# Performance work log

Measured on AMD Instinct MI355X. Metric: run time of the kernel, lower is better.

Reference implementation:

```python
import jax, jax.numpy as jnp
import numpy as np

B, L = 16, 256
H, NH, NL = 512, 8, 6
NTOK = 10000
P, K = 4, 9          # parser layers, conv kernel size
DFF = 4 * H


def layernorm(x, s=None, b=None, eps=1e-5):
    m = x.mean(-1, keepdims=True)
    v = ((x - m) ** 2).mean(-1, keepdims=True)
    y = (x - m) * jax.lax.rsqrt(v + eps)
    if s is not None:
        y = y * s + b
    return y


def conv1d(h, w, b):
    # h: (B,L,C); w: (K,Cin,Cout); 'same' padding (K odd)
    pad = (K - 1) // 2
    return jax.lax.conv_general_dilated(
        h, w, (1,), [(pad, pad)], dimension_numbers=('NWC', 'WIO', 'NWC')) + b


def setup_inputs():
    key = jax.random.key(0)
    ks = iter(jax.random.split(key, 40))
    r = lambda shape, s=0.02: jax.random.normal(next(ks), shape, jnp.float32) * s
    return dict(
        x=jax.random.randint(next(ks), (B, L), 0, NTOK, jnp.int32),
        pos=jnp.tile(jnp.arange(L, dtype=jnp.int32), (B, 1)),
        emb=r((NTOK, H), 0.1),
        conv_w=r((P, K, H, H)), conv_b=jnp.zeros((P, H)),
        parent_w=r((H, H)), parent_b=jnp.zeros((H,)),
        child_w=r((H, H)), child_b=jnp.zeros((H,)),
        rel_w_param=r((NL, NH, 2), 0.1),
        qkv_w=r((NL, 3 * H, H)), qkv_b=jnp.zeros((NL, 3 * H)),
        out_w=r((NL, H, H)), out_b=jnp.zeros((NL, H)),
        ln1_s=jnp.ones((NL, H)), ln1_b=jnp.zeros((NL, H)),
        ln2_s=jnp.ones((NL, H)), ln2_b=jnp.zeros((NL, H)),
        ff1_w=r((NL, DFF, H)), ff1_b=jnp.zeros((NL, DFF)),
        ff2_w=r((NL, H, DFF)), ff2_b=jnp.zeros((NL, H)),
        norm_s=jnp.ones((H,)), norm_b=jnp.zeros((H,)),
        out_bias=jnp.zeros((NTOK,)),
    )


def _forward(x, floats):
    (emb, conv_w, conv_b, parent_w, parent_b, child_w, child_b, rel_w_param,
     qkv_w, qkv_b, out_w, out_b, ln1_s, ln1_b, ln2_s, ln2_b,
     ff1_w, ff1_b, ff2_w, ff2_b, norm_s, norm_b, out_bias) = floats
    mask = x != 0  # pad token index = 0
    DH = H // NH
    scale = H ** -0.5
    # ---- differentiable parser: Conv1d + LN(no affine) + Tanh stack ----
    h = emb[x]
    for i in range(P):
        h = jnp.where(mask[..., None], h, 0.0)
        h = jnp.tanh(layernorm(conv1d(h, conv_w[i], conv_b[i])))
    parent = h @ parent_w.T + parent_b
    child = h @ child_w.T + child_b
    logits = jnp.einsum('bid,bjd->bij', child, parent) * scale
    logits = jnp.where(mask[:, None, :], logits, -jnp.inf)
    # NB: source applies scaling twice (masked_fill then softmax(logits*scaling))
    p = jax.nn.softmax(logits * scale, axis=-1)  # (B,L,L) head distribution
    # ---- structural relations -> per-layer/per-head attention bias ----
    eye = jnp.eye(L, dtype=bool)
    head = jnp.where(eye, 0.0, p)
    child_rel = jnp.swapaxes(head, 1, 2)
    rel = jnp.stack([head, child_rel], axis=1)            # (B,2,L,L)
    rel_weight = jax.nn.softmax(rel_w_param, axis=-1)     # (NL,NH,2)
    dep = jnp.einsum('lhr,brij->lbhij', rel_weight, rel)  # (NL,B,NH,L,L)
    # ---- pre-LN transformer encoder with structural bias injection ----
    logvis = jnp.where(mask, 0.0, -jnp.inf)[:, None, None, :]  # key padding mask (log)
    h = emb[x]
    for i in range(NL):
        hn = layernorm(h, ln1_s[i], ln1_b[i])
        qkv = hn @ qkv_w[i].T + qkv_b[i]
        q, k, v = jnp.split(qkv, 3, axis=-1)
        split = lambda t: t.reshape(B, L, NH, DH).transpose(0, 2, 1, 3)
        q, k, v = split(q), split(k), split(v)
        att = jnp.einsum('bhid,bhjd->bhij', q, k) * (DH ** -0.5) + dep[i] + logvis
        att = jax.nn.softmax(att, axis=-1)
        ctx = jnp.einsum('bhij,bhjd->bhid', att, v).transpose(0, 2, 1, 3).reshape(B, L, H)
        h = h + ctx @ out_w[i].T + out_b[i]
        hn = layernorm(h, ln2_s[i], ln2_b[i])
        h = h + jax.nn.leaky_relu(hn @ ff1_w[i].T + ff1_b[i], 0.01) @ ff2_w[i].T + ff2_b[i]
    raw = layernorm(h, norm_s, norm_b)
    out = (raw @ emb.T + out_bias).reshape(B * L, NTOK)  # tied output embedding
    return out


def reference(x, pos, emb, conv_w, conv_b, parent_w, parent_b, child_w, child_b,
              rel_w_param, qkv_w, qkv_b, out_w, out_b, ln1_s, ln1_b, ln2_s, ln2_b,
              ff1_w, ff1_b, ff2_w, ff2_b, norm_s, norm_b, out_bias):
    floats = (emb, conv_w, conv_b, parent_w, parent_b, child_w, child_b, rel_w_param,
              qkv_w, qkv_b, out_w, out_b, ln1_s, ln1_b, ln2_s, ln2_b,
              ff1_w, ff1_b, ff2_w, ff2_b, norm_s, norm_b, out_bias)
    return _forward(x, floats)
```

## Files before the change

kernel.cpp:

```cpp
#include <hip/hip_runtime.h>
#include <hip/hip_bf16.h>


typedef unsigned short u16;
typedef unsigned char  u8;
typedef short short8 __attribute__((ext_vector_type(8)));
typedef float f32x4  __attribute__((ext_vector_type(4)));

static constexpr int CB=16, CL=256, CH=512, CNH=8, CDH=64, CNL=6;
static constexpr int CNTOK=10000, CP=4, CKS=9, CDFF=2048, CT=CB*CL;

__device__ __forceinline__ u16 f2b(float x){
    union { float f; unsigned u; } v; v.f = x;
    unsigned r = v.u + 0x7fffu + ((v.u >> 16) & 1u);
    return (u16)(r >> 16);
}
__device__ __forceinline__ float b2f(u16 u){
    union { unsigned u; float f; } v; v.u = ((unsigned)u) << 16; return v.f;
}
__device__ __forceinline__ unsigned pack2(float a, float b){
    return (unsigned)f2b(a) | ((unsigned)f2b(b) << 16);
}

template<bool OBF>
__global__ __launch_bounds__(256) void embed_k(const int* __restrict__ x,
    const float* __restrict__ emb, void* __restrict__ out, u8* __restrict__ mask)
{
    int t = blockIdx.x, tid = threadIdx.x;
    int tok = x[t];
    if (tid == 0) mask[t] = (tok != 0) ? 1 : 0;
    const float* e = emb + (size_t)tok * CH;
    if (OBF) {
        u16* o = (u16*)out + (size_t)t * CH;
        o[tid] = f2b(e[tid]); o[tid + 256] = f2b(e[tid + 256]);
    } else {
        float* o = (float*)out + (size_t)t * CH;
        o[tid] = e[tid]; o[tid + 256] = e[tid + 256];
    }
}

template<bool INBF, bool AFFINE, bool DOTANH>
__global__ __launch_bounds__(256) void ln_k(const void* __restrict__ in,
    const float* __restrict__ s, const float* __restrict__ b, u16* __restrict__ out)
{
    int t = blockIdx.x, tid = threadIdx.x;
    float x0, x1;
    if (INBF) {
        const u16* row = (const u16*)in + (size_t)t * CH;
        x0 = b2f(row[tid]); x1 = b2f(row[tid + 256]);
    } else {
        const float* row = (const float*)in + (size_t)t * CH;
        x0 = row[tid]; x1 = row[tid + 256];
    }
    float sum = x0 + x1, sq = x0*x0 + x1*x1;
    #pragma unroll
    for (int o = 32; o; o >>= 1) { sum += __shfl_down(sum, o); sq += __shfl_down(sq, o); }
    __shared__ float rs[4], rq[4];
    int w = tid >> 6, lane = tid & 63;
    if (lane == 0) { rs[w] = sum; rq[w] = sq; }
    __syncthreads();
    sum = rs[0] + rs[1] + rs[2] + rs[3];
    sq  = rq[0] + rq[1] + rq[2] + rq[3];
    float mean = sum * (1.f/512.f);
    float var  = fmaxf(sq * (1.f/512.f) - mean*mean, 0.f);
    float rstd = rsqrtf(var + 1e-5f);
    float y0 = (x0 - mean) * rstd, y1 = (x1 - mean) * rstd;
    if (AFFINE) {
        y0 = y0 * s[tid]       + b[tid];
        y1 = y1 * s[tid + 256] + b[tid + 256];
    }
    if (DOTANH) { y0 = tanhf(y0); y1 = tanhf(y1); }
    u16* o = out + (size_t)t * CH;
    o[tid] = f2b(y0); o[tid + 256] = f2b(y1);
}

__global__ __launch_bounds__(256) void tp_conv(const float* __restrict__ src,
    u16* __restrict__ dst)
{
    __shared__ float tile[32][33];
    int z = blockIdx.z, p = z / 9, t = z % 9;
    int ci0 = blockIdx.y * 32, co0 = blockIdx.x * 32;
    int tx = threadIdx.x, ty = threadIdx.y;
    #pragma unroll
    for (int yy = 0; yy < 4; yy++) {
        int i = ty + yy*8;
        tile[i][tx] = src[((size_t)z*512 + ci0 + i)*512 + co0 + tx];
    }
    __syncthreads();
    #pragma unroll
    for (int yy = 0; yy < 4; yy++) {
        int i = ty + yy*8;
        dst[((size_t)p*512 + co0 + i)*4608 + (size_t)t*512 + ci0 + tx] = f2b(tile[tx][i]);
    }
}

template<bool CONV, int BSRC, int ACT, int OUT, int BMT>
__global__ __launch_bounds__(256) void gemm_mfma(
    const u16* __restrict__ A, const void* __restrict__ Bv,
    const float* __restrict__ bias, void* __restrict__ Cv,
    const u8* __restrict__ mask,
    int M, int N, int K, float alpha, long sA, long sB, long sC)
{
    constexpr int BM = BMT, MI = BMT/32;
    __shared__ __align__(16) u16 Al[4][BM][8];
    __shared__ __align__(16) u16 Bl[4][128][8];
    const int tid  = threadIdx.x;
    const int lane = tid & 63, wave = tid >> 6;
    const int q = lane >> 4, ln = lane & 15;
    const int wm = wave >> 1, wn = wave & 1;
    const int m0 = blockIdx.y * BM, n0 = blockIdx.x * 128;
    const int z  = blockIdx.z;
    A += (size_t)z * sA;

    f32x4 acc[MI][4];
    #pragma unroll
    for (int i = 0; i < MI; i++)
        #pragma unroll
        for (int j = 0; j < 4; j++)
            #pragma unroll
            for (int r = 0; r < 4; r++) acc[i][j][r] = 0.f;

    int ar, ak;
    if (BMT == 128) { ar = tid >> 1; ak = (tid & 1) * 16; }
    else            { ar = tid >> 2; ak = (tid & 3) * 8;  }
    const int br = tid >> 1, bk = (tid & 1) * 16;
    const int bn = n0 + br;

    const float* Bf = (const float*)Bv;
    const u16*   Bb = (const u16*)Bv;
    if (BSRC == 0) Bf += (size_t)z * sB; else Bb += (size_t)z * sB;

    for (int k0 = 0; k0 < K; k0 += 32) {
        {
            int row = m0 + ar;
            const u16* src;
            bool ok = true;
            if (CONV) {
                int koff = k0 >> 9;
                int ci   = (k0 & 511) + ak;
                int bb   = row >> 8;
                int l2   = (row & 255) + koff - 4;
                ok = ((unsigned)l2 < 256u) && mask[(bb << 8) | l2];
                src = A + ((size_t)((bb << 8) | l2)) * CH + ci;
            } else {
                src = A + (size_t)row * K + k0 + ak;
            }
            uint4 zv; zv.x = zv.y = zv.z = zv.w = 0u;
            if (BMT == 128) {
                uint4 v0 = ok ? *(const uint4*)src       : zv;
                uint4 v1 = ok ? *(const uint4*)(src + 8) : zv;
                int kq = (tid & 1) * 2;
                *(uint4*)&Al[kq][ar][0]     = v0;
                *(uint4*)&Al[kq + 1][ar][0] = v1;
            } else {
                uint4 v0 = ok ? *(const uint4*)src : zv;
                *(uint4*)&Al[tid & 3][ar][0] = v0;
            }
        }
        {
            uint4 w0, w1;
            w0.x = w0.y = w0.z = w0.w = 0u;
            w1 = w0;
            if (bn < N) {
                if (BSRC == 0) {
                    const float* s = Bf + (size_t)bn * K + k0 + bk;
                    float4 f0 = *(const float4*)s;
                    float4 f1 = *(const float4*)(s + 4);
                    float4 f2 = *(const float4*)(s + 8);
                    float4 f3 = *(const float4*)(s + 12);
                    w0.x = pack2(f0.x, f0.y); w0.y = pack2(f0.z, f0.w);
                    w0.z = pack2(f1.x, f1.y); w0.w = pack2(f1.z, f1.w);
                    w1.x = pack2(f2.x, f2.y); w1.y = pack2(f2.z, f2.w);
                    w1.z = pack2(f3.x, f3.y); w1.w = pack2(f3.z, f3.w);
                } else {
                    const u16* s = Bb + (size_t)bn * K + k0 + bk;
                    w0 = *(const uint4*)s;
                    w1 = *(const uint4*)(s + 8);
                }
            }
            int kq = (tid & 1) * 2;
            *(uint4*)&Bl[kq][br][0]     = w0;
            *(uint4*)&Bl[kq + 1][br][0] = w1;
        }
        __syncthreads();
        short8 af[MI], bf[4];
        #pragma unroll
        for (int i = 0; i < MI; i++)
            af[i] = *(const short8*)&Al[q][wm*(BM/2) + i*16 + ln][0];
        #pragma unroll
        for (int j = 0; j < 4; j++)
            bf[j] = *(const short8*)&Bl[q][wn*64 + j*16 + ln][0];
        #pragma unroll
        for (int i = 0; i < MI; i++)
            #pragma unroll
            for (int j = 0; j < 4; j++)
                acc[i][j] = __builtin_amdgcn_mfma_f32_16x16x32_bf16(af[i], bf[j], acc[i][j], 0, 0, 0);
        __syncthreads();
    }
    float* Cf = (float*)Cv; u16* Cb = (u16*)Cv;
    #pragma unroll
    for (int i = 0; i < MI; i++) {
        int row0 = m0 + wm*(BM/2) + i*16 + q*4;
        #pragma unroll
        for (int j = 0; j < 4; j++) {
            int col = n0 + wn*64 + j*16 + ln;
            if (col < N) {
                #pragma unroll
                for (int r = 0; r < 4; r++) {
                    float v = acc[i][j][r] * alpha;
                    if (bias) v += bias[col];
                    if (ACT == 1) v = v > 0.f ? v : 0.01f * v;
                    size_t idx = (size_t)z * sC + (size_t)(row0 + r) * N + col;
                    if (OUT == 0)      Cf[idx] = v;
                    else if (OUT == 1) Cb[idx] = f2b(v);
                    else               Cf[idx] += v;
                }
            }
        }
    }
}

__global__ __launch_bounds__(256) void softmax_head(float* __restrict__ sc,
    const u8* __restrict__ mask)
{
    int bi = blockIdx.x;
    int b = bi >> 8, i = bi & 255;
    int j = threadIdx.x;
    float* rowp = sc + (size_t)bi * CL;
    bool valid = mask[(b << 8) | j] != 0;
    float v = valid ? rowp[j] : -1e30f;
    float mx = v;
    #pragma unroll
    for (int o = 32; o; o >>= 1) mx = fmaxf(mx, __shfl_down(mx, o));
    __shared__ float rm[4], rsum[4];
    int w = j >> 6, lane = j & 63;
    if (lane == 0) rm[w] = mx;
    __syncthreads();
    mx = fmaxf(fmaxf(rm[0], rm[1]), fmaxf(rm[2], rm[3]));
    float e = valid ? __expf(v - mx) : 0.f;
    float ssum = e;
    #pragma unroll
    for (int o = 32; o; o >>= 1) ssum += __shfl_down(ssum, o);
    if (lane == 0) rsum[w] = ssum;
    __syncthreads();
    ssum = rsum[0] + rsum[1] + rsum[2] + rsum[3];
    float r = e / fmaxf(ssum, 1e-30f);
    if (j == i) r = 0.f;
    rowp[j] = r;
}

__global__ __launch_bounds__(256) void attn_k(const u16* __restrict__ qkv,
    const float* __restrict__ head, const float* __restrict__ relw,
    const u8* __restrict__ mask, u16* __restrict__ ctx, int layer)
{
    __shared__ __align__(16) u16 Ks[CL * CDH];
    __shared__ __align__(16) u16 Vs[CL * CDH];
    int bx = blockIdx.x;
    int b = bx >> 4, hd = (bx >> 1) & 7, qh = bx & 1;
    int tid = threadIdx.x;

    #pragma unroll
    for (int r = 0; r < 8; r++) {
        int ef = tid + 256 * r;
        int j = ef >> 3, d8 = (ef & 7) * 8;
        const u16* ps = qkv + (size_t)(b*256 + j) * 1536 + 512 + hd*64 + d8;
        *(uint4*)&Ks[j*64 + d8] = *(const uint4*)ps;
        *(uint4*)&Vs[j*64 + d8] = *(const uint4*)(ps + 512);
    }

    int qi = qh * 128 + (tid >> 1);
    int half = tid & 1;
    float qv[CDH];
    {
        const u16* qp = qkv + (size_t)(b*256 + qi) * 1536 + hd*64;
        #pragma unroll
        for (int c = 0; c < 8; c++) {
            uint4 u = *(const uint4*)(qp + c*8);
            unsigned uu[4] = {u.x, u.y, u.z, u.w};
            #pragma unroll
            for (int p2 = 0; p2 < 4; p2++) {
                qv[c*8 + p2*2]     = b2f((u16)(uu[p2] & 0xffffu));
                qv[c*8 + p2*2 + 1] = b2f((u16)(uu[p2] >> 16));
            }
        }
    }
    float r0 = relw[((layer << 3) + hd) * 2 + 0];
    float r1 = relw[((layer << 3) + hd) * 2 + 1];
    float e0 = __expf(r0), e1 = __expf(r1);
    float w0 = e0 / (e0 + e1), w1 = 1.f - w0;

    __syncthreads();

    const float* h1 = head + ((size_t)b << 16) + ((size_t)qi << 8);
    const float* h2 = head + ((size_t)b << 16) + qi;
    const u8* mb = mask + (b << 8);

    float m = -1e30f, lsum = 0.f;
    float acc[CDH];
    #pragma unroll
    for (int d = 0; d < CDH; d++) acc[d] = 0.f;

    for (int jj = 0; jj < 128; jj++) {
        int j = half * 128 + jj;
        if (!mb[j]) continue;
        float dot = 0.f;
        #pragma unroll
        for (int d = 0; d < CDH; d++) dot += qv[d] * b2f(Ks[(j << 6) + d]);
        float s = dot * 0.125f + w0 * h1[j] + w1 * h2[(size_t)j << 8];
        float mn = fmaxf(m, s);
        float c = __expf(m - mn);
        float p = __expf(s - mn);
        lsum = lsum * c + p;
        #pragma unroll
        for (int d = 0; d < CDH; d++) acc[d] = acc[d] * c + p * b2f(Vs[(j << 6) + d]);
        m = mn;
    }
    {
        float mo = __shfl_xor(m, 1);
        float lo = __shfl_xor(lsum, 1);
        float M  = fmaxf(m, mo);
        float cs = __expf(m - M);
        float co = __expf(mo - M);
        lsum = lsum * cs + lo * co;
        #pragma unroll
        for (int d = 0; d < CDH; d++) {
            float ao = __shfl_xor(acc[d], 1);
            acc[d] = acc[d] * cs + ao * co;
        }
    }
    if (half == 0) {
        float inv = 1.f / fmaxf(lsum, 1e-30f);
        u16* cp = ctx + (size_t)(b*256 + qi) * CH + (hd << 6);
        #pragma unroll
        for (int d = 0; d < CDH; d++) cp[d] = f2b(acc[d] * inv);
    }
}

extern "C" void kernel_launch(void* const* d_in, const int* in_sizes, int n_in,
                              void* d_out, int out_size, void* d_ws, size_t ws_size,
                              hipStream_t stream)
{
    const int*   x        = (const int*)d_in[0];
    const float* emb      = (const float*)d_in[2];
    const float* conv_w   = (const float*)d_in[3];
    const float* conv_b   = (const float*)d_in[4];
    const float* parent_w = (const float*)d_in[5];
    const float* parent_b = (const float*)d_in[6];
    const float* child_w  = (const float*)d_in[7];
    const float* child_b  = (const float*)d_in[8];
    const float* rel_w    = (const float*)d_in[9];
    const float* qkv_w    = (const float*)d_in[10];
    const float* qkv_b    = (const float*)d_in[11];
    const float* out_w    = (const float*)d_in[12];
    const float* out_b    = (const float*)d_in[13];
    const float* ln1_s    = (const float*)d_in[14];
    const float* ln1_b    = (const float*)d_in[15];
    const float* ln2_s    = (const float*)d_in[16];
    const float* ln2_b    = (const float*)d_in[17];
    const float* ff1_w    = (const float*)d_in[18];
    const float* ff1_b    = (const float*)d_in[19];
    const float* ff2_w    = (const float*)d_in[20];
    const float* ff2_b    = (const float*)d_in[21];
    const float* norm_s   = (const float*)d_in[22];
    const float* norm_b   = (const float*)d_in[23];
    const float* out_bias = (const float*)d_in[24];

    float* ws = (float*)d_ws;
    float* h      = ws;
    float* headp  = ws + 2097152;
    u16*   abuf   = (u16*)(ws + 3145728);
    u16*   Rb     = (u16*)(ws + 4194304);
    u16*   qkvb   = Rb;
    u16*   parentb= Rb;
    u16*   childb = Rb + 2097152;
    u16*   convo  = Rb + 4194304;
    u16*   ctxb   = (u16*)(ws + 7340032);
    u16*   ff1b   = (u16*)(ws + 8388608);
    u16*   convwb = (u16*)(ws + 7340032);
    u8*    maskb  = (u8*)(ws + 12582912);

    tp_conv<<<dim3(16,16,36), dim3(32,8), 0, stream>>>(conv_w, convwb);

    embed_k<true><<<CT, 256, 0, stream>>>(x, emb, abuf, maskb);
    for (int p = 0; p < CP; p++) {
        gemm_mfma<true,1,0,1,64><<<dim3(4,64,1), 256, 0, stream>>>(
            abuf, convwb + (size_t)p*512*4608, conv_b + p*512, convo, maskb,
            CT, 512, 4608, 1.f, 0, 0, 0);
        ln_k<true,false,true><<<CT, 256, 0, stream>>>(convo, nullptr, nullptr, abuf);
    }
    gemm_mfma<false,0,0,1,64><<<dim3(4,64,1), 256, 0, stream>>>(
        abuf, parent_w, parent_b, parentb, nullptr, CT, 512, 512, 1.f, 0, 0, 0);
    gemm_mfma<false,0,0,1,64><<<dim3(4,64,1), 256, 0, stream>>>(
        abuf, child_w, child_b, childb, nullptr, CT, 512, 512, 1.f, 0, 0, 0);
    gemm_mfma<false,1,0,0,64><<<dim3(2,4,16), 256, 0, stream>>>(
        childb, parentb, nullptr, headp, nullptr, 256, 256, 512, 1.f/512.f,
        131072, 131072, 65536);
    softmax_head<<<CT, 256, 0, stream>>>(headp, maskb);

    embed_k<false><<<CT, 256, 0, stream>>>(x, emb, h, maskb);
    for (int l = 0; l < CNL; l++) {
        ln_k<false,true,false><<<CT, 256, 0, stream>>>(h, ln1_s + l*CH, ln1_b + l*CH, abuf);
        gemm_mfma<false,0,0,1,128><<<dim3(12,32,1), 256, 0, stream>>>(
            abuf, qkv_w + (size_t)l*1536*512, qkv_b + l*1536, qkvb, nullptr,
            CT, 1536, 512, 1.f, 0, 0, 0);
        attn_k<<<256, 256, 0, stream>>>(qkvb, headp, rel_w, maskb, ctxb, l);
        gemm_mfma<false,0,0,2,64><<<dim3(4,64,1), 256, 0, stream>>>(
            ctxb, out_w + (size_t)l*512*512, out_b + l*512, h, nullptr,
            CT, 512, 512, 1.f, 0, 0, 0);
        ln_k<false,true,false><<<CT, 256, 0, stream>>>(h, ln2_s + l*CH, ln2_b + l*CH, abuf);
        gemm_mfma<false,0,1,1,128><<<dim3(16,32,1), 256, 0, stream>>>(
            abuf, ff1_w + (size_t)l*2048*512, ff1_b + l*2048, ff1b, nullptr,
            CT, 2048, 512, 1.f, 0, 0, 0);
        gemm_mfma<false,0,0,2,64><<<dim3(4,64,1), 256, 0, stream>>>(
            ff1b, ff2_w + (size_t)l*512*2048, ff2_b + l*512, h, nullptr,
            CT, 512, 2048, 1.f, 0, 0, 0);
    }
    ln_k<false,true,false><<<CT, 256, 0, stream>>>(h, norm_s, norm_b, abuf);
    gemm_mfma<false,0,0,0,128><<<dim3(79,32,1), 256, 0, stream>>>(
        abuf, emb, out_bias, d_out, nullptr, CT, CNTOK, 512, 1.f, 0, 0, 0);
}
```

Before: 2.900 ms.

## Pre-convert weights to bf16 and load GEMM tiles via global_load_lds

Adds conversion kernels that turn all fp32 weight matrices and the tied embedding into bf16 copies once per call, padding the embedding to a multiple of 128 rows. The GEMM kernel is rewritten to stage A and B tiles straight into LDS with global_load_lds, replacing the register round trip and the per-tile fp32-to-bf16 packing. It also merges the two embedding gathers into one kernel and adds an optional workgroup swizzle, used for the output projection. The cost is extra conversion launches and extra memory traffic for the weight copies on every call.

```diff
diff --git a/kernel.cpp b/kernel.cpp
--- a/kernel.cpp
+++ b/kernel.cpp
@@ -9,6 +9,7 @@
 
 static constexpr int CB=16, CL=256, CH=512, CNH=8, CDH=64, CNL=6;
 static constexpr int CNTOK=10000, CP=4, CKS=9, CDFF=2048, CT=CB*CL;
+static constexpr int NTOKP=10112;
 
 __device__ __forceinline__ u16 f2b(float x){
     union { float f; unsigned u; } v; v.f = x;
@@ -21,22 +22,40 @@
 __device__ __forceinline__ unsigned pack2(float a, float b){
     return (unsigned)f2b(a) | ((unsigned)f2b(b) << 16);
 }
-
-template<bool OBF>
-__global__ __launch_bounds__(256) void embed_k(const int* __restrict__ x,
-    const float* __restrict__ emb, void* __restrict__ out, u8* __restrict__ mask)
+__device__ __forceinline__ void gll16(const void* g, void* l){
+    __builtin_amdgcn_global_load_lds(
+        (__attribute__((address_space(1))) void*)g,
+        (__attribute__((address_space(3))) void*)l, 16, 0, 0);
+}
+
+__global__ __launch_bounds__(256) void cvt_k(const float* __restrict__ in,
+    u16* __restrict__ out, long n, long total)
+{
+    long i = ((long)blockIdx.x * 256 + threadIdx.x) * 8;
+    if (i >= total) return;
+    uint4 o;
+    if (i < n) {
+        float4 a = *(const float4*)(in + i);
+        float4 b = *(const float4*)(in + i + 4);
+        o.x = pack2(a.x, a.y); o.y = pack2(a.z, a.w);
+        o.z = pack2(b.x, b.y); o.w = pack2(b.z, b.w);
+    } else { o.x = o.y = o.z = o.w = 0u; }
+    *(uint4*)(out + i) = o;
+}
+
+__global__ __launch_bounds__(256) void embed2_k(const int* __restrict__ x,
+    const float* __restrict__ emb, float* __restrict__ h,
+    u16* __restrict__ abuf, u8* __restrict__ maskb)
 {
     int t = blockIdx.x, tid = threadIdx.x;
     int tok = x[t];
-    if (tid == 0) mask[t] = (tok != 0) ? 1 : 0;
+    if (tid == 0) maskb[t] = (tok != 0) ? 1 : 0;
     const float* e = emb + (size_t)tok * CH;
-    if (OBF) {
-        u16* o = (u16*)out + (size_t)t * CH;
-        o[tid] = f2b(e[tid]); o[tid + 256] = f2b(e[tid + 256]);
-    } else {
-        float* o = (float*)out + (size_t)t * CH;
-        o[tid] = e[tid]; o[tid + 256] = e[tid + 256];
-    }
+    float v0 = e[tid], v1 = e[tid + 256];
+    float* hp = h + (size_t)t * CH;
+    hp[tid] = v0; hp[tid + 256] = v1;
+    u16* ap = abuf + (size_t)t * CH;
+    ap[tid] = f2b(v0); ap[tid + 256] = f2b(v1);
 }
 
 template<bool INBF, bool AFFINE, bool DOTANH>
@@ -94,23 +113,31 @@
     }
 }
 
-template<bool CONV, int BSRC, int ACT, int OUT, int BMT>
-__global__ __launch_bounds__(256) void gemm_mfma(
-    const u16* __restrict__ A, const void* __restrict__ Bv,
+template<int BM, bool CONV, int ACT, int OUT>
+__global__ __launch_bounds__(256) void gemm2(
+    const u16* __restrict__ A, const u16* __restrict__ B,
     const float* __restrict__ bias, void* __restrict__ Cv,
     const u8* __restrict__ mask,
-    int M, int N, int K, float alpha, long sA, long sB, long sC)
-{
-    constexpr int BM = BMT, MI = BMT/32;
-    __shared__ __align__(16) u16 Al[4][BM][8];
-    __shared__ __align__(16) u16 Bl[4][128][8];
+    int M, int N, int K, float alpha, long sA, long sB, long sC, int swz)
+{
+    constexpr int MI = BM / 32;
+    __shared__ __align__(16) u16 As[32 * BM];
+    __shared__ __align__(16) u16 Bs[4096];
+
+    int bx = blockIdx.x, by = blockIdx.y;
+    if (swz) {
+        int nwg = gridDim.x * gridDim.y;
+        int bid = by * gridDim.x + bx;
+        int s = (bid & 7) * (nwg >> 3) + (bid >> 3);
+        bx = s % gridDim.x; by = s / gridDim.x;
+    }
     const int tid  = threadIdx.x;
     const int lane = tid & 63, wave = tid >> 6;
     const int q = lane >> 4, ln = lane & 15;
     const int wm = wave >> 1, wn = wave & 1;
-    const int m0 = blockIdx.y * BM, n0 = blockIdx.x * 128;
+    const int m0 = by * BM, n0 = bx * 128;
     const int z  = blockIdx.z;
-    A += (size_t)z * sA;
+    A += (size_t)z * sA; B += (size_t)z * sB;
 
     f32x4 acc[MI][4];
     #pragma unroll
@@ -120,94 +147,61 @@
             #pragma unroll
             for (int r = 0; r < 4; r++) acc[i][j][r] = 0.f;
 
-    int ar, ak;
-    if (BMT == 128) { ar = tid >> 1; ak = (tid & 1) * 16; }
-    else            { ar = tid >> 2; ak = (tid & 3) * 8;  }
-    const int br = tid >> 1, bk = (tid & 1) * 16;
-    const int bn = n0 + br;
-
-    const float* Bf = (const float*)Bv;
-    const u16*   Bb = (const u16*)Bv;
-    if (BSRC == 0) Bf += (size_t)z * sB; else Bb += (size_t)z * sB;
-
     for (int k0 = 0; k0 < K; k0 += 32) {
-        {
-            int row = m0 + ar;
-            const u16* src;
-            bool ok = true;
-            if (CONV) {
-                int koff = k0 >> 9;
-                int ci   = (k0 & 511) + ak;
-                int bb   = row >> 8;
-                int l2   = (row & 255) + koff - 4;
-                ok = ((unsigned)l2 < 256u) && mask[(bb << 8) | l2];
-                src = A + ((size_t)((bb << 8) | l2)) * CH + ci;
+        if (!CONV) {
+            if (BM == 128) {
+                #pragma unroll
+                for (int t = 0; t < 2; t++) {
+                    int c = wave + t*4;
+                    int kq = c >> 1, rh = (c & 1) << 6;
+                    gll16(A + (size_t)(m0 + rh + lane) * K + k0 + kq*8, As + c*512);
+                }
             } else {
-                src = A + (size_t)row * K + k0 + ak;
+                gll16(A + (size_t)(m0 + lane) * K + k0 + wave*8, As + wave*512);
             }
-            uint4 zv; zv.x = zv.y = zv.z = zv.w = 0u;
-            if (BMT == 128) {
-                uint4 v0 = ok ? *(const uint4*)src       : zv;
-                uint4 v1 = ok ? *(const uint4*)(src + 8) : zv;
-                int kq = (tid & 1) * 2;
-                *(uint4*)&Al[kq][ar][0]     = v0;
-                *(uint4*)&Al[kq + 1][ar][0] = v1;
-            } else {
-                uint4 v0 = ok ? *(const uint4*)src : zv;
-                *(uint4*)&Al[tid & 3][ar][0] = v0;
-            }
+        } else {
+            int tap = k0 >> 9;
+            int ci  = (k0 & 511) + wave*8;
+            int gr  = m0 + lane;
+            int bb  = gr >> 8;
+            int l2  = (gr & 255) + tap - 4;
+            bool ok = ((unsigned)l2 < 256u) && mask[(bb << 8) | l2];
+            uint4 v; v.x = v.y = v.z = v.w = 0u;
+            if (ok) v = *(const uint4*)(A + ((size_t)((bb << 8) | l2)) * CH + ci);
+            *(uint4*)&As[wave*512 + lane*8] = v;
         }
-        {
-            uint4 w0, w1;
-            w0.x = w0.y = w0.z = w0.w = 0u;
-            w1 = w0;
-            if (bn < N) {
-                if (BSRC == 0) {
-                    const float* s = Bf + (size_t)bn * K + k0 + bk;
-                    float4 f0 = *(const float4*)s;
-                    float4 f1 = *(const float4*)(s + 4);
-                    float4 f2 = *(const float4*)(s + 8);
-                    float4 f3 = *(const float4*)(s + 12);
-                    w0.x = pack2(f0.x, f0.y); w0.y = pack2(f0.z, f0.w);
-                    w0.z = pack2(f1.x, f1.y); w0.w = pack2(f1.z, f1.w);
-                    w1.x = pack2(f2.x, f2.y); w1.y = pack2(f2.z, f2.w);
-                    w1.z = pack2(f3.x, f3.y); w1.w = pack2(f3.z, f3.w);
-                } else {
-                    const u16* s = Bb + (size_t)bn * K + k0 + bk;
-                    w0 = *(const uint4*)s;
-                    w1 = *(const uint4*)(s + 8);
-                }
-            }
-            int kq = (tid & 1) * 2;
-            *(uint4*)&Bl[kq][br][0]     = w0;
-            *(uint4*)&Bl[kq + 1][br][0] = w1;
+        #pragma unroll
+        for (int t = 0; t < 2; t++) {
+            int c = wave + t*4;
+            int kq = c >> 1, rh = (c & 1) << 6;
+            gll16(B + (size_t)(n0 + rh + lane) * K + k0 + kq*8, Bs + c*512);
         }
         __syncthreads();
         short8 af[MI], bf[4];
         #pragma unroll
-        for (int i = 0; i < MI; i++)
-            af[i] = *(const short8*)&Al[q][wm*(BM/2) + i*16 + ln][0];
-        #pragma unroll
-        for (int j = 0; j < 4; j++)
-            bf[j] = *(const short8*)&Bl[q][wn*64 + j*16 + ln][0];
-        #pragma unroll
-        for (int i = 0; i < MI; i++)
+        for (int f = 0; f < MI; f++)
+            af[f] = *(const short8*)&As[q*(BM*8) + (wm*(BM/2) + f*16 + ln)*8];
+        #pragma unroll
+        for (int g = 0; g < 4; g++)
+            bf[g] = *(const short8*)&Bs[q*1024 + (wn*64 + g*16 + ln)*8];
+        #pragma unroll
+        for (int f = 0; f < MI; f++)
             #pragma unroll
-            for (int j = 0; j < 4; j++)
-                acc[i][j] = __builtin_amdgcn_mfma_f32_16x16x32_bf16(af[i], bf[j], acc[i][j], 0, 0, 0);
+            for (int g = 0; g < 4; g++)
+                acc[f][g] = __builtin_amdgcn_mfma_f32_16x16x32_bf16(af[f], bf[g], acc[f][g], 0, 0, 0);
         __syncthreads();
     }
     float* Cf = (float*)Cv; u16* Cb = (u16*)Cv;
     #pragma unroll
-    for (int i = 0; i < MI; i++) {
-        int row0 = m0 + wm*(BM/2) + i*16 + q*4;
-        #pragma unroll
-        for (int j = 0; j < 4; j++) {
-            int col = n0 + wn*64 + j*16 + ln;
+    for (int f = 0; f < MI; f++) {
+        int row0 = m0 + wm*(BM/2) + f*16 + q*4;
+        #pragma unroll
+        for (int g = 0; g < 4; g++) {
+            int col = n0 + wn*64 + g*16 + ln;
             if (col < N) {
                 #pragma unroll
                 for (int r = 0; r < 4; r++) {
-                    float v = acc[i][j][r] * alpha;
+                    float v = acc[f][g][r] * alpha;
                     if (bias) v += bias[col];
                     if (ACT == 1) v = v > 0.f ? v : 0.01f * v;
                     size_t idx = (size_t)z * sC + (size_t)(row0 + r) * N + col;
@@ -378,44 +372,58 @@
     u16*   ff1b   = (u16*)(ws + 8388608);
     u16*   convwb = (u16*)(ws + 7340032);
     u8*    maskb  = (u8*)(ws + 12582912);
+    u16*   ebf16  = (u16*)(ws + 12583936);
+    u16*   qkvwb  = (u16*)(ws + 15172608);
+    u16*   outwb  = (u16*)(ws + 17531904);
+    u16*   ff1wb  = (u16*)(ws + 18318336);
+    u16*   ff2wb  = (u16*)(ws + 21464064);
+    u16*   parwb  = (u16*)(ws + 24609792);
+    u16*   chlwb  = (u16*)(ws + 24740864);
 
     tp_conv<<<dim3(16,16,36), dim3(32,8), 0, stream>>>(conv_w, convwb);
-
-    embed_k<true><<<CT, 256, 0, stream>>>(x, emb, abuf, maskb);
+    cvt_k<<<2528, 256, 0, stream>>>(emb,      ebf16, (long)CNTOK*CH, (long)NTOKP*CH);
+    cvt_k<<<2304, 256, 0, stream>>>(qkv_w,    qkvwb, 4718592L, 4718592L);
+    cvt_k<<< 768, 256, 0, stream>>>(out_w,    outwb, 1572864L, 1572864L);
+    cvt_k<<<3072, 256, 0, stream>>>(ff1_w,    ff1wb, 6291456L, 6291456L);
+    cvt_k<<<3072, 256, 0, stream>>>(ff2_w,    ff2wb, 6291456L, 6291456L);
+    cvt_k<<< 128, 256, 0, stream>>>(parent_w, parwb,  262144L,  262144L);
+    cvt_k<<< 128, 256, 0, stream>>>(child_w,  chlwb,  262144L,  262144L);
+
+    embed2_k<<<CT, 256, 0, stream>>>(x, emb, h, abuf, maskb);
+
     for (int p = 0; p < CP; p++) {
-        gemm_mfma<true,1,0,1,64><<<dim3(4,64,1), 256, 0, stream>>>(
+        gemm2<64,true,0,1><<<dim3(4,64,1), 256, 0, stream>>>(
             abuf, convwb + (size_t)p*512*4608, conv_b + p*512, convo, maskb,
-            CT, 512, 4608, 1.f, 0, 0, 0);
+            CT, 512, 4608, 1.f, 0, 0, 0, 0);
         ln_k<true,false,true><<<CT, 256, 0, stream>>>(convo, nullptr, nullptr, abuf);
     }
-    gemm_mfma<false,0,0,1,64><<<dim3(4,64,1), 256, 0, stream>>>(
-        abuf, parent_w, parent_b, parentb, nullptr, CT, 512, 512, 1.f, 0, 0, 0);
-    gemm_mfma<false,0,0,1,64><<<dim3(4,64,1), 256, 0, stream>>>(
-        abuf, child_w, child_b, childb, nullptr, CT, 512, 512, 1.f, 0, 0, 0);
-    gemm_mfma<false,1,0,0,64><<<dim3(2,4,16), 256, 0, stream>>>(
+    gemm2<64,false,0,1><<<dim3(4,64,1), 256, 0, stream>>>(
+        abuf, parwb, parent_b, parentb, nullptr, CT, 512, 512, 1.f, 0, 0, 0, 0);
+    gemm2<64,false,0,1><<<dim3(4,64,1), 256, 0, stream>>>(
+        abuf, chlwb, child_b, childb, nullptr, CT, 512, 512, 1.f, 0, 0, 0, 0);
+    gemm2<64,false,0,0><<<dim3(2,4,16), 256, 0, stream>>>(
         childb, parentb, nullptr, headp, nullptr, 256, 256, 512, 1.f/512.f,
-        131072, 131072, 65536);
+        131072, 131072, 65536, 0);
     softmax_head<<<CT, 256, 0, stream>>>(headp, maskb);
 
-    embed_k<false><<<CT, 256, 0, stream>>>(x, emb, h, maskb);
     for (int l = 0; l < CNL; l++) {
         ln_k<false,true,false><<<CT, 256, 0, stream>>>(h, ln1_s + l*CH, ln1_b + l*CH, abuf);
-        gemm_mfma<false,0,0,1,128><<<dim3(12,32,1), 256, 0, stream>>>(
-            abuf, qkv_w + (size_t)l*1536*512, qkv_b + l*1536, qkvb, nullptr,
-            CT, 1536, 512, 1.f, 0, 0, 0);
+        gemm2<128,false,0,1><<<dim3(12,32,1), 256, 0, stream>>>(
+            abuf, qkvwb + (size_t)l*1536*512, qkv_b + l*1536, qkvb, nullptr,
+            CT, 1536, 512, 1.f, 0, 0, 0, 0);
         attn_k<<<256, 256, 0, stream>>>(qkvb, headp, rel_w, maskb, ctxb, l);
-        gemm_mfma<false,0,0,2,64><<<dim3(4,64,1), 256, 0, stream>>>(
-            ctxb, out_w + (size_t)l*512*512, out_b + l*512, h, nullptr,
-            CT, 512, 512, 1.f, 0, 0, 0);
+        gemm2<64,false,0,2><<<dim3(4,64,1), 256, 0, stream>>>(
+            ctxb, outwb + (size_t)l*512*512, out_b + l*512, h, nullptr,
+            CT, 512, 512, 1.f, 0, 0, 0, 0);
         ln_k<false,true,false><<<CT, 256, 0, stream>>>(h, ln2_s + l*CH, ln2_b + l*CH, abuf);
-        gemm_mfma<false,0,1,1,128><<<dim3(16,32,1), 256, 0, stream>>>(
-            abuf, ff1_w + (size_t)l*2048*512, ff1_b + l*2048, ff1b, nullptr,
-            CT, 2048, 512, 1.f, 0, 0, 0);
-        gemm_mfma<false,0,0,2,64><<<dim3(4,64,1), 256, 0, stream>>>(
-            ff1b, ff2_w + (size_t)l*512*2048, ff2_b + l*512, h, nullptr,
-            CT, 512, 2048, 1.f, 0, 0, 0);
+        gemm2<128,false,1,1><<<dim3(16,32,1), 256, 0, stream>>>(
+            abuf, ff1wb + (size_t)l*2048*512, ff1_b + l*2048, ff1b, nullptr,
+            CT, 2048, 512, 1.f, 0, 0, 0, 0);
+        gemm2<64,false,0,2><<<dim3(4,64,1), 256, 0, stream>>>(
+            ff1b, ff2wb + (size_t)l*512*2048, ff2_b + l*512, h, nullptr,
+            CT, 512, 2048, 1.f, 0, 0, 0, 0);
     }
     ln_k<false,true,false><<<CT, 256, 0, stream>>>(h, norm_s, norm_b, abuf);
-    gemm_mfma<false,0,0,0,128><<<dim3(79,32,1), 256, 0, stream>>>(
-        abuf, emb, out_bias, d_out, nullptr, CT, CNTOK, 512, 1.f, 0, 0, 0);
-}
+    gemm2<128,false,0,0><<<dim3(79,32,1), 256, 0, stream>>>(
+        abuf, ebf16, out_bias, d_out, nullptr, CT, CNTOK, 512, 1.f, 0, 0, 0, 1);
+}
```

Measured after the change: 2.595 ms. 1.12x faster.
